# Performance work log

Measured on AMD Instinct MI355X. Metric: run time of the kernel, lower is better.

The kernel has to match this reference:

```python
import jax, jax.numpy as jnp
import numpy as np

H = 64  # hidden_size

def _lstm_last_hidden(x, w_ih, w_hh, b_ih, b_hh):
    # x: [B, T, D]; PyTorch gate order: i, f, g, o (each of size H)
    B, T, D = x.shape
    # Precompute input contribution for all timesteps: [T, B, 4H]
    xg = jnp.einsum('btd,gd->tbg', x, w_ih) + (b_ih + b_hh)

    def step(carry, xg_t):
        h, c = carry
        gates = xg_t + h @ w_hh.T  # [B, 4H]
        i = jax.nn.sigmoid(gates[:, 0*H:1*H])
        f = jax.nn.sigmoid(gates[:, 1*H:2*H])
        g = jnp.tanh(gates[:, 2*H:3*H])
        o = jax.nn.sigmoid(gates[:, 3*H:4*H])
        c = f * c + i * g
        h = o * jnp.tanh(c)
        return (h, c), None

    h0 = jnp.zeros((B, H), dtype=x.dtype)
    c0 = jnp.zeros((B, H), dtype=x.dtype)
    (h_last, _), _ = jax.lax.scan(step, (h0, c0), xg)
    return h_last  # [B, H] == hidden[:, -1, :]


def setup_inputs() -> dict:
    key = jax.random.key(0)
    ks = jax.random.split(key, 8)
    B, T, D, OUT = 256, 2048, 64, 8
    s = 1.0 / np.sqrt(H)  # PyTorch LSTM init scale
    return {
        'x':    jax.random.normal(ks[0], (B, T, D), dtype=jnp.float32),
        'w_ih': jax.random.uniform(ks[1], (4 * H, D), minval=-s, maxval=s, dtype=jnp.float32),
        'w_hh': jax.random.uniform(ks[2], (4 * H, H), minval=-s, maxval=s, dtype=jnp.float32),
        'b_ih': jax.random.uniform(ks[3], (4 * H,), minval=-s, maxval=s, dtype=jnp.float32),
        'b_hh': jax.random.uniform(ks[4], (4 * H,), minval=-s, maxval=s, dtype=jnp.float32),
        'fc_w': jax.random.uniform(ks[5], (OUT, H), minval=-s, maxval=s, dtype=jnp.float32),
        'fc_b': jax.random.uniform(ks[6], (OUT,), minval=-s, maxval=s, dtype=jnp.float32),
    }


def reference(x, w_ih, w_hh, b_ih, b_hh, fc_w, fc_b):
    h_last = _lstm_last_hidden(x, w_ih, w_hh, b_ih, b_hh)  # [B, H]
    return h_last @ fc_w.T + fc_b  # [B, OUT]
```

## Files before the change

### kernel.cpp

```cpp
#include <hip/hip_runtime.h>
#include <math.h>


#define Hh 64
#define Tt 2048
#define Bb 256
#define OUTN 8
#define CHUNK 64
#define NCHUNK (Tt / CHUNK)

typedef float floatx4 __attribute__((ext_vector_type(4)));
typedef float floatx2 __attribute__((ext_vector_type(2)));

__device__ __forceinline__ float hsum4(floatx4 a) {
    floatx2 t = a.lo + a.hi;
    return t.x + t.y;
}

__device__ __forceinline__ float sigm2(float zp) {
    return __builtin_amdgcn_rcpf(1.0f + __builtin_amdgcn_exp2f(zp));
}

__global__ __launch_bounds__(256, 1)
void lstm_fused_kernel(const float* __restrict__ x,
                       const float* __restrict__ w_ih,
                       const float* __restrict__ w_hh,
                       const float* __restrict__ b_ih,
                       const float* __restrict__ b_hh,
                       const float* __restrict__ fc_w,
                       const float* __restrict__ fc_b,
                       float* __restrict__ out)
{
    __shared__ __align__(16) float xch[2][CHUNK * Hh];
    __shared__ __align__(16) float P[2][4][Hh][4];
    __shared__ __align__(16) float h_s[Hh];

    const int tid  = threadIdx.x;
    const int b    = blockIdx.x;
    const int wave = tid >> 6;
    const int lane = tid & 63;

    const float* xb = x + (size_t)b * Tt * Hh;

    const float SC1 = -1.44269504088896340736f;
    const float SC2 = -2.88539008177792681472f;

    floatx4 wx[4][4], wh[4][4];
    {
        const int kb = 16 * wave;
        #pragma unroll
        for (int g = 0; g < 4; ++g) {
            const float sc = (g == 2) ? SC2 : SC1;
            const floatx4* pi = (const floatx4*)(w_ih + (size_t)((g << 6) + lane) * Hh + kb);
            const floatx4* ph = (const floatx4*)(w_hh + (size_t)((g << 6) + lane) * Hh + kb);
            #pragma unroll
            for (int q = 0; q < 4; ++q) { wx[g][q] = pi[q] * sc; wh[g][q] = ph[q] * sc; }
        }
        #pragma unroll
        for (int g = 0; g < 4; ++g)
            #pragma unroll
            for (int q = 0; q < 4; ++q)
                asm volatile("" : "+v"(wx[g][q]), "+v"(wh[g][q]));
    }
    floatx4 bias4;
    bias4.x = (b_ih[lane]       + b_hh[lane])       * SC1;
    bias4.y = (b_ih[64 + lane]  + b_hh[64 + lane])  * SC1;
    bias4.z = (b_ih[128 + lane] + b_hh[128 + lane]) * SC2;
    bias4.w = (b_ih[192 + lane] + b_hh[192 + lane]) * SC1;

    #pragma unroll
    for (int p4 = 0; p4 < 4; ++p4) {
        __builtin_amdgcn_global_load_lds(
            (const __attribute__((address_space(1))) void*)(xb + p4 * 1024 + tid * 4),
            (__attribute__((address_space(3))) void*)(&xch[0][p4 * 1024 + tid * 4]),
            16, 0, 0);
    }
    if (tid < Hh) h_s[tid] = 0.0f;
    float c = 0.0f;
    __syncthreads();

    floatx4 acc0, acc1, acc2, acc3;
    {
        const floatx4* xs = (const floatx4*)(&xch[0][16 * wave]);
        floatx4 v = xs[0];
        acc0 = wx[0][0] * v; acc1 = wx[1][0] * v;
        acc2 = wx[2][0] * v; acc3 = wx[3][0] * v;
        #pragma unroll
        for (int q = 1; q < 4; ++q) {
            v = xs[q];
            acc0 = __builtin_elementwise_fma(wx[0][q], v, acc0);
            acc1 = __builtin_elementwise_fma(wx[1][q], v, acc1);
            acc2 = __builtin_elementwise_fma(wx[2][q], v, acc2);
            acc3 = __builtin_elementwise_fma(wx[3][q], v, acc3);
        }
    }

    for (int cc = 0; cc < NCHUNK; ++cc) {
        const float* xcbuf = &xch[cc & 1][0];

        #pragma unroll 2
        for (int s = 0; s < CHUNK; ++s) {
            const int par = s & 1;

            const floatx4* hs4 = (const floatx4*)(h_s + 16 * wave);
            #pragma unroll
            for (int q = 0; q < 4; ++q) {
                floatx4 v = hs4[q];
                acc0 = __builtin_elementwise_fma(wh[0][q], v, acc0);
                acc1 = __builtin_elementwise_fma(wh[1][q], v, acc1);
                acc2 = __builtin_elementwise_fma(wh[2][q], v, acc2);
                acc3 = __builtin_elementwise_fma(wh[3][q], v, acc3);
            }
            floatx4 part;
            part.x = hsum4(acc0); part.y = hsum4(acc1);
            part.z = hsum4(acc2); part.w = hsum4(acc3);
            *(floatx4*)&P[par][wave][lane][0] = part;
            __syncthreads();

            if (s == 0 && cc + 1 < NCHUNK) {
                const float* src = xb + (size_t)(cc + 1) * CHUNK * Hh;
                float* dst = &xch[(cc + 1) & 1][0];
                #pragma unroll
                for (int p4 = 0; p4 < 4; ++p4) {
                    __builtin_amdgcn_global_load_lds(
                        (const __attribute__((address_space(1))) void*)(src + p4 * 1024 + tid * 4),
                        (__attribute__((address_space(3))) void*)(dst + p4 * 1024 + tid * 4),
                        16, 0, 0);
                }
            }

            floatx4 p0 = *(const floatx4*)&P[par][0][lane][0];
            floatx4 p1 = *(const floatx4*)&P[par][1][lane][0];
            floatx4 p2 = *(const floatx4*)&P[par][2][lane][0];
            floatx4 p3 = *(const floatx4*)&P[par][3][lane][0];

            const float* xn = (s + 1 < CHUNK) ? (xcbuf + (s + 1) * Hh)
                                              : &xch[(cc + 1) & 1][0];
            const floatx4* xs = (const floatx4*)(xn + 16 * wave);
            floatx4 n0, n1, n2, n3;
            {
                floatx4 v = xs[0];
                n0 = wx[0][0] * v; n1 = wx[1][0] * v;
                n2 = wx[2][0] * v; n3 = wx[3][0] * v;
            }
            #pragma unroll
            for (int q = 1; q < 4; ++q) {
                floatx4 v = xs[q];
                n0 = __builtin_elementwise_fma(wx[0][q], v, n0);
                n1 = __builtin_elementwise_fma(wx[1][q], v, n1);
                n2 = __builtin_elementwise_fma(wx[2][q], v, n2);
                n3 = __builtin_elementwise_fma(wx[3][q], v, n3);
            }

            floatx4 z = bias4 + ((p0 + p1) + (p2 + p3));
            float i_ = sigm2(z.x);
            float f_ = sigm2(z.y);
            float g_ = 2.0f * sigm2(z.z) - 1.0f;
            float o_ = sigm2(z.w);
            c = __builtin_fmaf(f_, c, i_ * g_);
            float th = 2.0f * sigm2(SC2 * c) - 1.0f;
            h_s[lane] = o_ * th;

            acc0 = n0; acc1 = n1; acc2 = n2; acc3 = n3;
        }
    }
    __syncthreads();

    if (tid < OUTN) {
        float acc = fc_b[tid];
        #pragma unroll
        for (int j = 0; j < Hh; ++j) acc += fc_w[tid * Hh + j] * h_s[j];
        out[b * OUTN + tid] = acc;
    }
}

extern "C" void kernel_launch(void* const* d_in, const int* in_sizes, int n_in,
                              void* d_out, int out_size, void* d_ws, size_t ws_size,
                              hipStream_t stream) {
    const float* x    = (const float*)d_in[0];
    const float* w_ih = (const float*)d_in[1];
    const float* w_hh = (const float*)d_in[2];
    const float* b_ih = (const float*)d_in[3];
    const float* b_hh = (const float*)d_in[4];
    const float* fc_w = (const float*)d_in[5];
    const float* fc_b = (const float*)d_in[6];
    float* out = (float*)d_out;

    lstm_fused_kernel<<<Bb, 256, 0, stream>>>(x, w_ih, w_hh, b_ih, b_hh,
                                              fc_w, fc_b, out);
}
```

Before: 993.3 us.

## Split LSTM into producer wave for input gates and single consumer recurrence wave

Replaces the four-wave design, which cross-reduced partial gate sums through LDS with a block barrier every timestep. Now one producer wave stages x chunks and precomputes the input projection plus bias into an LDS ring. A single consumer wave holds all of w_hh in registers and runs the full 64-wide recurrent dot per step with no per-step barrier, syncing only once per 16-step chunk. The trade-off is that the serial per-step FMA work on one wave is four times larger, and each wave now keeps a 256-register weight array.

Measured after the change: 2.265 ms. 128% more time.

```diff
diff --git a/kernel.cpp b/kernel.cpp
--- a/kernel.cpp
+++ b/kernel.cpp
@@ -6,8 +6,8 @@
 #define Tt 2048
 #define Bb 256
 #define OUTN 8
-#define CHUNK 64
-#define NCHUNK (Tt / CHUNK)
+#define CH 16
+#define NCHUNKS (Tt / CH)
 
 typedef float floatx4 __attribute__((ext_vector_type(4)));
 typedef float floatx2 __attribute__((ext_vector_type(2)));
@@ -21,156 +21,148 @@
     return __builtin_amdgcn_rcpf(1.0f + __builtin_amdgcn_exp2f(zp));
 }
 
-__global__ __launch_bounds__(256, 1)
-void lstm_fused_kernel(const float* __restrict__ x,
-                       const float* __restrict__ w_ih,
-                       const float* __restrict__ w_hh,
-                       const float* __restrict__ b_ih,
-                       const float* __restrict__ b_hh,
-                       const float* __restrict__ fc_w,
-                       const float* __restrict__ fc_b,
-                       float* __restrict__ out)
+__global__ __launch_bounds__(128, 1)
+void lstm_pc_kernel(const float* __restrict__ x,
+                    const float* __restrict__ w_ih,
+                    const float* __restrict__ w_hh,
+                    const float* __restrict__ b_ih,
+                    const float* __restrict__ b_hh,
+                    const float* __restrict__ fc_w,
+                    const float* __restrict__ fc_b,
+                    float* __restrict__ out)
 {
-    __shared__ __align__(16) float xch[2][CHUNK * Hh];
-    __shared__ __align__(16) float P[2][4][Hh][4];
+    __shared__ __align__(16) float ring[2][CH][Hh][4];
+    __shared__ __align__(16) float xst[2][CH][Hh];
     __shared__ __align__(16) float h_s[Hh];
 
     const int tid  = threadIdx.x;
     const int b    = blockIdx.x;
     const int wave = tid >> 6;
     const int lane = tid & 63;
-
     const float* xb = x + (size_t)b * Tt * Hh;
 
     const float SC1 = -1.44269504088896340736f;
     const float SC2 = -2.88539008177792681472f;
 
-    floatx4 wx[4][4], wh[4][4];
+    floatx4 w[4][16];
     {
-        const int kb = 16 * wave;
+        const float* wp = (wave == 1) ? w_ih : w_hh;
         #pragma unroll
         for (int g = 0; g < 4; ++g) {
             const float sc = (g == 2) ? SC2 : SC1;
-            const floatx4* pi = (const floatx4*)(w_ih + (size_t)((g << 6) + lane) * Hh + kb);
-            const floatx4* ph = (const floatx4*)(w_hh + (size_t)((g << 6) + lane) * Hh + kb);
+            const floatx4* p = (const floatx4*)(wp + (size_t)((g << 6) + lane) * Hh);
             #pragma unroll
-            for (int q = 0; q < 4; ++q) { wx[g][q] = pi[q] * sc; wh[g][q] = ph[q] * sc; }
+            for (int q = 0; q < 16; ++q) w[g][q] = p[q] * sc;
         }
         #pragma unroll
         for (int g = 0; g < 4; ++g)
             #pragma unroll
-            for (int q = 0; q < 4; ++q)
-                asm volatile("" : "+v"(wx[g][q]), "+v"(wh[g][q]));
+            for (int q = 0; q < 16; ++q)
+                asm volatile("" : "+v"(w[g][q]));
     }
+
     floatx4 bias4;
     bias4.x = (b_ih[lane]       + b_hh[lane])       * SC1;
     bias4.y = (b_ih[64 + lane]  + b_hh[64 + lane])  * SC1;
     bias4.z = (b_ih[128 + lane] + b_hh[128 + lane]) * SC2;
     bias4.w = (b_ih[192 + lane] + b_hh[192 + lane]) * SC1;
 
-    #pragma unroll
-    for (int p4 = 0; p4 < 4; ++p4) {
-        __builtin_amdgcn_global_load_lds(
-            (const __attribute__((address_space(1))) void*)(xb + p4 * 1024 + tid * 4),
-            (__attribute__((address_space(3))) void*)(&xch[0][p4 * 1024 + tid * 4]),
-            16, 0, 0);
+    auto stage_chunk = [&](int xbuf, int chunk) {
+        const float* src = xb + (size_t)chunk * CH * Hh;
+        float* dst = &xst[xbuf][0][0];
+        #pragma unroll
+        for (int p4 = 0; p4 < 4; ++p4)
+            __builtin_amdgcn_global_load_lds(
+                (const __attribute__((address_space(1))) void*)(src + p4 * 256 + lane * 4),
+                (__attribute__((address_space(3))) void*)(dst + p4 * 256 + lane * 4),
+                16, 0, 0);
+    };
+
+    auto produce_chunk = [&](int rbuf, const float* xc) {
+        for (int s = 0; s < CH; ++s) {
+            const floatx4* xs = (const floatx4*)(xc + s * Hh);
+            floatx4 a0, a1, a2, a3;
+            {
+                floatx4 v = xs[0];
+                a0 = w[0][0] * v; a1 = w[1][0] * v;
+                a2 = w[2][0] * v; a3 = w[3][0] * v;
+            }
+            #pragma unroll
+            for (int q = 1; q < 16; ++q) {
+                floatx4 v = xs[q];
+                a0 = __builtin_elementwise_fma(w[0][q], v, a0);
+                a1 = __builtin_elementwise_fma(w[1][q], v, a1);
+                a2 = __builtin_elementwise_fma(w[2][q], v, a2);
+                a3 = __builtin_elementwise_fma(w[3][q], v, a3);
+            }
+            floatx4 xg;
+            xg.x = hsum4(a0); xg.y = hsum4(a1);
+            xg.z = hsum4(a2); xg.w = hsum4(a3);
+            xg += bias4;
+            *(floatx4*)&ring[rbuf][s][lane][0] = xg;
+        }
+    };
+
+    if (wave == 1) {
+        stage_chunk(0, 0);
+        stage_chunk(1, 1);
+        asm volatile("s_waitcnt vmcnt(4)" ::: "memory");
+        __builtin_amdgcn_sched_barrier(0);
+        produce_chunk(0, &xst[0][0][0]);
+    } else {
+        h_s[lane] = 0.0f;
     }
-    if (tid < Hh) h_s[tid] = 0.0f;
+
     float c = 0.0f;
-    __syncthreads();
 
-    floatx4 acc0, acc1, acc2, acc3;
-    {
-        const floatx4* xs = (const floatx4*)(&xch[0][16 * wave]);
-        floatx4 v = xs[0];
-        acc0 = wx[0][0] * v; acc1 = wx[1][0] * v;
-        acc2 = wx[2][0] * v; acc3 = wx[3][0] * v;
-        #pragma unroll
-        for (int q = 1; q < 4; ++q) {
-            v = xs[q];
-            acc0 = __builtin_elementwise_fma(wx[0][q], v, acc0);
-            acc1 = __builtin_elementwise_fma(wx[1][q], v, acc1);
-            acc2 = __builtin_elementwise_fma(wx[2][q], v, acc2);
-            acc3 = __builtin_elementwise_fma(wx[3][q], v, acc3);
+    for (int cc = 0; cc < NCHUNKS; ++cc) {
+        __syncthreads();
+
+        if (wave == 1) {
+            if (cc + 2 < NCHUNKS) stage_chunk(cc & 1, cc + 2);
+            if (cc + 1 < NCHUNKS) produce_chunk((cc + 1) & 1, &xst[(cc + 1) & 1][0][0]);
+            asm volatile("s_waitcnt vmcnt(0)" ::: "memory");
+        } else {
+            #pragma unroll 2
+            for (int s = 0; s < CH; ++s) {
+                floatx4 xg = *(const floatx4*)&ring[cc & 1][s][lane][0];
+
+                const floatx4* hs4 = (const floatx4*)h_s;
+                floatx4 a0, a1, a2, a3;
+                {
+                    floatx4 v = hs4[0];
+                    a0 = w[0][0] * v; a1 = w[1][0] * v;
+                    a2 = w[2][0] * v; a3 = w[3][0] * v;
+                }
+                #pragma unroll
+                for (int q = 1; q < 16; ++q) {
+                    floatx4 v = hs4[q];
+                    a0 = __builtin_elementwise_fma(w[0][q], v, a0);
+                    a1 = __builtin_elementwise_fma(w[1][q], v, a1);
+                    a2 = __builtin_elementwise_fma(w[2][q], v, a2);
+                    a3 = __builtin_elementwise_fma(w[3][q], v, a3);
+                }
+                floatx4 z;
+                z.x = hsum4(a0); z.y = hsum4(a1);
+                z.z = hsum4(a2); z.w = hsum4(a3);
+                z += xg;
+
+                float i_ = sigm2(z.x);
+                float f_ = sigm2(z.y);
+                float g_ = 2.0f * sigm2(z.z) - 1.0f;
+                float o_ = sigm2(z.w);
+                c = __builtin_fmaf(f_, c, i_ * g_);
+                float th = 2.0f * sigm2(SC2 * c) - 1.0f;
+                h_s[lane] = o_ * th;
+            }
         }
     }
 
-    for (int cc = 0; cc < NCHUNK; ++cc) {
-        const float* xcbuf = &xch[cc & 1][0];
-
-        #pragma unroll 2
-        for (int s = 0; s < CHUNK; ++s) {
-            const int par = s & 1;
-
-            const floatx4* hs4 = (const floatx4*)(h_s + 16 * wave);
-            #pragma unroll
-            for (int q = 0; q < 4; ++q) {
-                floatx4 v = hs4[q];
-                acc0 = __builtin_elementwise_fma(wh[0][q], v, acc0);
-                acc1 = __builtin_elementwise_fma(wh[1][q], v, acc1);
-                acc2 = __builtin_elementwise_fma(wh[2][q], v, acc2);
-                acc3 = __builtin_elementwise_fma(wh[3][q], v, acc3);
-            }
-            floatx4 part;
-            part.x = hsum4(acc0); part.y = hsum4(acc1);
-            part.z = hsum4(acc2); part.w = hsum4(acc3);
-            *(floatx4*)&P[par][wave][lane][0] = part;
-            __syncthreads();
-
-            if (s == 0 && cc + 1 < NCHUNK) {
-                const float* src = xb + (size_t)(cc + 1) * CHUNK * Hh;
-                float* dst = &xch[(cc + 1) & 1][0];
-                #pragma unroll
-                for (int p4 = 0; p4 < 4; ++p4) {
-                    __builtin_amdgcn_global_load_lds(
-                        (const __attribute__((address_space(1))) void*)(src + p4 * 1024 + tid * 4),
-                        (__attribute__((address_space(3))) void*)(dst + p4 * 1024 + tid * 4),
-                        16, 0, 0);
-                }
-            }
-
-            floatx4 p0 = *(const floatx4*)&P[par][0][lane][0];
-            floatx4 p1 = *(const floatx4*)&P[par][1][lane][0];
-            floatx4 p2 = *(const floatx4*)&P[par][2][lane][0];
-            floatx4 p3 = *(const floatx4*)&P[par][3][lane][0];
-
-            const float* xn = (s + 1 < CHUNK) ? (xcbuf + (s + 1) * Hh)
-                                              : &xch[(cc + 1) & 1][0];
-            const floatx4* xs = (const floatx4*)(xn + 16 * wave);
-            floatx4 n0, n1, n2, n3;
-            {
-                floatx4 v = xs[0];
-                n0 = wx[0][0] * v; n1 = wx[1][0] * v;
-                n2 = wx[2][0] * v; n3 = wx[3][0] * v;
-            }
-            #pragma unroll
-            for (int q = 1; q < 4; ++q) {
-                floatx4 v = xs[q];
-                n0 = __builtin_elementwise_fma(wx[0][q], v, n0);
-                n1 = __builtin_elementwise_fma(wx[1][q], v, n1);
-                n2 = __builtin_elementwise_fma(wx[2][q], v, n2);
-                n3 = __builtin_elementwise_fma(wx[3][q], v, n3);
-            }
-
-            floatx4 z = bias4 + ((p0 + p1) + (p2 + p3));
-            float i_ = sigm2(z.x);
-            float f_ = sigm2(z.y);
-            float g_ = 2.0f * sigm2(z.z) - 1.0f;
-            float o_ = sigm2(z.w);
-            c = __builtin_fmaf(f_, c, i_ * g_);
-            float th = 2.0f * sigm2(SC2 * c) - 1.0f;
-            h_s[lane] = o_ * th;
-
-            acc0 = n0; acc1 = n1; acc2 = n2; acc3 = n3;
-        }
-    }
-    __syncthreads();
-
-    if (tid < OUTN) {
-        float acc = fc_b[tid];
+    if (wave == 0 && lane < OUTN) {
+        float acc = fc_b[lane];
         #pragma unroll
-        for (int j = 0; j < Hh; ++j) acc += fc_w[tid * Hh + j] * h_s[j];
-        out[b * OUTN + tid] = acc;
+        for (int j = 0; j < Hh; ++j) acc += fc_w[lane * Hh + j] * h_s[j];
+        out[b * OUTN + lane] = acc;
     }
 }
 
@@ -186,6 +178,6 @@
     const float* fc_b = (const float*)d_in[6];
     float* out = (float*)d_out;
 
-    lstm_fused_kernel<<<Bb, 256, 0, stream>>>(x, w_ih, w_hh, b_ih, b_hh,
-                                              fc_w, fc_b, out);
+    lstm_pc_kernel<<<Bb, 128, 0, stream>>>(x, w_ih, w_hh, b_ih, b_hh,
+                                           fc_w, fc_b, out);
 }
```

## Broadcast hidden state via readlane and prefetch x into registers

Applied to the files above, without the earlier changes.

Removes the LDS chunk staging of x and the h_s shared-memory round trip. Each wave now recomputes the full hidden vector redundantly and broadcasts it to its lanes with readlane, and prefetches x rows a few timesteps ahead directly into registers. The __syncthreads is replaced by a raw s_waitcnt+s_barrier. This cuts LDS traffic and one shared write/read on the recurrence critical path. In exchange it costs 16 readlanes per step and more register pressure.

New measurement: 1.283 ms. 1.29x slower.

```diff
diff --git a/kernel.cpp b/kernel.cpp
--- a/kernel.cpp
+++ b/kernel.cpp
@@ -6,8 +6,6 @@
 #define Tt 2048
 #define Bb 256
 #define OUTN 8
-#define CHUNK 64
-#define NCHUNK (Tt / CHUNK)
 
 typedef float floatx4 __attribute__((ext_vector_type(4)));
 typedef float floatx2 __attribute__((ext_vector_type(2)));
@@ -20,6 +18,76 @@
 __device__ __forceinline__ float sigm2(float zp) {
     return __builtin_amdgcn_rcpf(1.0f + __builtin_amdgcn_exp2f(zp));
 }
+
+#define LSTM_STEP(T_, PAR_, BUF_)                                            \
+  {                                                                          \
+       \
+    _Pragma("unroll")                                                        \
+    for (int q = 0; q < 4; ++q) {                                            \
+      floatx4 v = hv[q];                                                     \
+      acc0 = __builtin_elementwise_fma(wh[0][q], v, acc0);                   \
+      acc1 = __builtin_elementwise_fma(wh[1][q], v, acc1);                   \
+      acc2 = __builtin_elementwise_fma(wh[2][q], v, acc2);                   \
+      acc3 = __builtin_elementwise_fma(wh[3][q], v, acc3);                   \
+    }                                                                        \
+    floatx4 part;                                                            \
+    part.x = hsum4(acc0); part.y = hsum4(acc1);                              \
+    part.z = hsum4(acc2); part.w = hsum4(acc3);                              \
+    *(floatx4*)&P[PAR_][wave][lane][0] = part;                               \
+      \
+    asm volatile("s_waitcnt lgkmcnt(0)\n\ts_barrier" ::: "memory");          \
+         \
+    floatx4 p0 = *(const floatx4*)&P[PAR_][0][lane][0];                      \
+    floatx4 p1 = *(const floatx4*)&P[PAR_][1][lane][0];                      \
+    floatx4 p2 = *(const floatx4*)&P[PAR_][2][lane][0];                      \
+    floatx4 p3 = *(const floatx4*)&P[PAR_][3][lane][0];                      \
+    \
+    floatx4 n0, n1, n2, n3;                                                  \
+    {                                                                        \
+      floatx4 v = BUF_[0];                                                   \
+      n0 = wx[0][0] * v; n1 = wx[1][0] * v;                                  \
+      n2 = wx[2][0] * v; n3 = wx[3][0] * v;                                  \
+    }                                                                        \
+    _Pragma("unroll")                                                        \
+    for (int q = 1; q < 4; ++q) {                                            \
+      floatx4 v = BUF_[q];                                                   \
+      n0 = __builtin_elementwise_fma(wx[0][q], v, n0);                       \
+      n1 = __builtin_elementwise_fma(wx[1][q], v, n1);                       \
+      n2 = __builtin_elementwise_fma(wx[2][q], v, n2);                       \
+      n3 = __builtin_elementwise_fma(wx[3][q], v, n3);                       \
+    }                                                                        \
+    \
+    {                                                                        \
+      int tn = (T_) + 3; if (tn > Tt - 1) tn = Tt - 1;                       \
+      unsigned voff = (unsigned)(tn * (Hh * 4) + (kb16 << 2));               \
+      asm volatile("" : "+v"(voff));               \
+      const floatx4* xp = (const floatx4*)((const char*)xb + voff);          \
+      _Pragma("unroll")                                                      \
+      for (int q = 0; q < 4; ++q) BUF_[q] = xp[q];                           \
+    }                                                                        \
+        \
+    floatx4 z = bias4 + ((p0 + p1) + (p2 + p3));                             \
+    float i_ = sigm2(z.x);                                                   \
+    float f_ = sigm2(z.y);                                                   \
+    float g_ = 2.0f * sigm2(z.z) - 1.0f;             \
+    float o_ = sigm2(z.w);                                                   \
+    c = __builtin_fmaf(f_, c, i_ * g_);                                      \
+    float th = 2.0f * sigm2(SC2 * c) - 1.0f;                                 \
+    hj = o_ * th;                                                            \
+      \
+    {                                                                        \
+      const int hbits = __float_as_int(hj);                                  \
+      _Pragma("unroll")                                                      \
+      for (int q = 0; q < 4; ++q) {                                          \
+        _Pragma("unroll")                                                    \
+        for (int e = 0; e < 4; ++e) {                                        \
+          hv[q][e] = __int_as_float(                                         \
+              __builtin_amdgcn_readlane(hbits, kb16 + 4 * q + e));           \
+        }                                                                    \
+      }                                                                      \
+    }                                                                        \
+    acc0 = n0; acc1 = n1; acc2 = n2; acc3 = n3;                              \
+  }
 
 __global__ __launch_bounds__(256, 1)
 void lstm_fused_kernel(const float* __restrict__ x,
@@ -31,7 +99,6 @@
                        const float* __restrict__ fc_b,
                        float* __restrict__ out)
 {
-    __shared__ __align__(16) float xch[2][CHUNK * Hh];
     __shared__ __align__(16) float P[2][4][Hh][4];
     __shared__ __align__(16) float h_s[Hh];
 
@@ -46,13 +113,13 @@
     const float SC2 = -2.88539008177792681472f;
 
     floatx4 wx[4][4], wh[4][4];
+    const int kb16 = 16 * wave;
     {
-        const int kb = 16 * wave;
         #pragma unroll
         for (int g = 0; g < 4; ++g) {
             const float sc = (g == 2) ? SC2 : SC1;
-            const floatx4* pi = (const floatx4*)(w_ih + (size_t)((g << 6) + lane) * Hh + kb);
-            const floatx4* ph = (const floatx4*)(w_hh + (size_t)((g << 6) + lane) * Hh + kb);
+            const floatx4* pi = (const floatx4*)(w_ih + (size_t)((g << 6) + lane) * Hh + kb16);
+            const floatx4* ph = (const floatx4*)(w_hh + (size_t)((g << 6) + lane) * Hh + kb16);
             #pragma unroll
             for (int q = 0; q < 4; ++q) { wx[g][q] = pi[q] * sc; wh[g][q] = ph[q] * sc; }
         }
@@ -68,26 +135,42 @@
     bias4.z = (b_ih[128 + lane] + b_hh[128 + lane]) * SC2;
     bias4.w = (b_ih[192 + lane] + b_hh[192 + lane]) * SC1;
 
+    floatx4 bA[4], bB[4];
+    floatx4 x0[4];
+    {
+        unsigned v0 = (unsigned)(kb16 << 2);
+        asm volatile("" : "+v"(v0));
+        const floatx4* xp0 = (const floatx4*)((const char*)xb + v0);
+        #pragma unroll
+        for (int q = 0; q < 4; ++q) x0[q] = xp0[q];
+
+        unsigned v1 = (unsigned)(1 * (Hh * 4) + (kb16 << 2));
+        asm volatile("" : "+v"(v1));
+        const floatx4* xp1 = (const floatx4*)((const char*)xb + v1);
+        #pragma unroll
+        for (int q = 0; q < 4; ++q) bA[q] = xp1[q];
+
+        unsigned v2 = (unsigned)(2 * (Hh * 4) + (kb16 << 2));
+        asm volatile("" : "+v"(v2));
+        const floatx4* xp2 = (const floatx4*)((const char*)xb + v2);
+        #pragma unroll
+        for (int q = 0; q < 4; ++q) bB[q] = xp2[q];
+    }
+
+    float c = 0.0f;
+    float hj = 0.0f;
+    floatx4 hv[4];
     #pragma unroll
-    for (int p4 = 0; p4 < 4; ++p4) {
-        __builtin_amdgcn_global_load_lds(
-            (const __attribute__((address_space(1))) void*)(xb + p4 * 1024 + tid * 4),
-            (__attribute__((address_space(3))) void*)(&xch[0][p4 * 1024 + tid * 4]),
-            16, 0, 0);
-    }
-    if (tid < Hh) h_s[tid] = 0.0f;
-    float c = 0.0f;
-    __syncthreads();
+    for (int q = 0; q < 4; ++q) hv[q] = (floatx4)(0.0f);
 
     floatx4 acc0, acc1, acc2, acc3;
     {
-        const floatx4* xs = (const floatx4*)(&xch[0][16 * wave]);
-        floatx4 v = xs[0];
+        floatx4 v = x0[0];
         acc0 = wx[0][0] * v; acc1 = wx[1][0] * v;
         acc2 = wx[2][0] * v; acc3 = wx[3][0] * v;
         #pragma unroll
         for (int q = 1; q < 4; ++q) {
-            v = xs[q];
+            v = x0[q];
             acc0 = __builtin_elementwise_fma(wx[0][q], v, acc0);
             acc1 = __builtin_elementwise_fma(wx[1][q], v, acc1);
             acc2 = __builtin_elementwise_fma(wx[2][q], v, acc2);
@@ -95,77 +178,13 @@
         }
     }
 
-    for (int cc = 0; cc < NCHUNK; ++cc) {
-        const float* xcbuf = &xch[cc & 1][0];
-
-        #pragma unroll 2
-        for (int s = 0; s < CHUNK; ++s) {
-            const int par = s & 1;
-
-            const floatx4* hs4 = (const floatx4*)(h_s + 16 * wave);
-            #pragma unroll
-            for (int q = 0; q < 4; ++q) {
-                floatx4 v = hs4[q];
-                acc0 = __builtin_elementwise_fma(wh[0][q], v, acc0);
-                acc1 = __builtin_elementwise_fma(wh[1][q], v, acc1);
-                acc2 = __builtin_elementwise_fma(wh[2][q], v, acc2);
-                acc3 = __builtin_elementwise_fma(wh[3][q], v, acc3);
-            }
-            floatx4 part;
-            part.x = hsum4(acc0); part.y = hsum4(acc1);
-            part.z = hsum4(acc2); part.w = hsum4(acc3);
-            *(floatx4*)&P[par][wave][lane][0] = part;
-            __syncthreads();
-
-            if (s == 0 && cc + 1 < NCHUNK) {
-                const float* src = xb + (size_t)(cc + 1) * CHUNK * Hh;
-                float* dst = &xch[(cc + 1) & 1][0];
-                #pragma unroll
-                for (int p4 = 0; p4 < 4; ++p4) {
-                    __builtin_amdgcn_global_load_lds(
-                        (const __attribute__((address_space(1))) void*)(src + p4 * 1024 + tid * 4),
-                        (__attribute__((address_space(3))) void*)(dst + p4 * 1024 + tid * 4),
-                        16, 0, 0);
-                }
-            }
-
-            floatx4 p0 = *(const floatx4*)&P[par][0][lane][0];
-            floatx4 p1 = *(const floatx4*)&P[par][1][lane][0];
-            floatx4 p2 = *(const floatx4*)&P[par][2][lane][0];
-            floatx4 p3 = *(const floatx4*)&P[par][3][lane][0];
-
-            const float* xn = (s + 1 < CHUNK) ? (xcbuf + (s + 1) * Hh)
-                                              : &xch[(cc + 1) & 1][0];
-            const floatx4* xs = (const floatx4*)(xn + 16 * wave);
-            floatx4 n0, n1, n2, n3;
-            {
-                floatx4 v = xs[0];
-                n0 = wx[0][0] * v; n1 = wx[1][0] * v;
-                n2 = wx[2][0] * v; n3 = wx[3][0] * v;
-            }
-            #pragma unroll
-            for (int q = 1; q < 4; ++q) {
-                floatx4 v = xs[q];
-                n0 = __builtin_elementwise_fma(wx[0][q], v, n0);
-                n1 = __builtin_elementwise_fma(wx[1][q], v, n1);
-                n2 = __builtin_elementwise_fma(wx[2][q], v, n2);
-                n3 = __builtin_elementwise_fma(wx[3][q], v, n3);
-            }
-
-            floatx4 z = bias4 + ((p0 + p1) + (p2 + p3));
-            float i_ = sigm2(z.x);
-            float f_ = sigm2(z.y);
-            float g_ = 2.0f * sigm2(z.z) - 1.0f;
-            float o_ = sigm2(z.w);
-            c = __builtin_fmaf(f_, c, i_ * g_);
-            float th = 2.0f * sigm2(SC2 * c) - 1.0f;
-            h_s[lane] = o_ * th;
-
-            acc0 = n0; acc1 = n1; acc2 = n2; acc3 = n3;
-        }
-    }
+    for (int t = 0; t < Tt; t += 2) {
+        LSTM_STEP(t,     0, bA)
+        LSTM_STEP(t + 1, 1, bB)
+    }
+
+    if (wave == 0) h_s[lane] = hj;
     __syncthreads();
-
     if (tid < OUTN) {
         float acc = fc_b[tid];
         #pragma unroll
```
